# Performance work log

Hardware: AMD Instinct MI355X
Metric: run time of the kernel (lower is better)

## Reference

```python
import jax, jax.numpy as jnp
import numpy as np

N_NODES, N_EDGES, WIDTH = 50000, 640000, 128


def setup_inputs() -> dict:
    key = jax.random.key(0)
    k1, k2, k3 = jax.random.split(key, 3)
    x = jax.random.normal(k1, (N_NODES, WIDTH), dtype=jnp.float32)
    e = jax.random.randint(k2, (2, N_EDGES), 0, N_NODES, dtype=jnp.int32)
    # LinearBlock(2*width, width): Linear(256 -> 128) + ReLU
    W = jax.random.normal(k3, (WIDTH, 2 * WIDTH), dtype=jnp.float32) * (1.0 / np.sqrt(2 * WIDTH))
    b = jnp.zeros((WIDTH,), dtype=jnp.float32)
    return {"x": x, "e": e, "W": W, "b": b}


def reference(x, e, W, b):
    src, dst = e[0], e[1]
    # gather-subtract: diffs[k] = x[dst_k] - x[src_k]  -> [E, width]
    diffs = x[dst] - x[src]
    n = x.shape[0]
    # scatter_max over destination nodes; torch_scatter leaves empty segments at 0
    maxes = jax.ops.segment_max(diffs, dst, num_segments=n)  # [N, width]
    deg = jax.ops.segment_sum(jnp.ones((dst.shape[0],), jnp.float32), dst, num_segments=n)
    maxes = jnp.where((deg > 0)[:, None], maxes, 0.0)
    # LinearBlock (Linear + ReLU) on concat, then residual
    h = jnp.concatenate([x, maxes], axis=1)  # [N, 2*width]
    return x + jax.nn.relu(h @ W.T + b)
```

## Files before the change

### kernel.cpp

```cpp
#include <hip/hip_runtime.h>

#define WIDTH   128
#define NNODES  50000
#define NEDGES  640000
#define NTILES  3125
#define WLDS_STRIDE 264

#define RBLK    8
#define SSEG    8
#define RSZ     6250
#define SEG_I4  20000
#define C0      16
#define CAPB    128

#define BIN_BLOCKS  (RBLK * SSEG)
#define CVT_BLOCKS  782
#define GRID_PREP   (BIN_BLOCKS + CVT_BLOCKS + 1)

typedef __attribute__((ext_vector_type(8))) short         short8;
typedef __attribute__((ext_vector_type(4))) short         short4_t;
typedef __attribute__((ext_vector_type(4))) float         float4_t;
typedef __attribute__((ext_vector_type(8))) _Float16      half8_t;
typedef __attribute__((ext_vector_type(2))) _Float16      h2v;
typedef __attribute__((ext_vector_type(2))) unsigned int  uint2v;

union H8 { short8 s; half8_t h; };

__device__ inline short f2bf(float f) {
    union { float f; unsigned int u; } a;
    a.f = f;
    unsigned int r = a.u + 0x7FFFu + ((a.u >> 16) & 1u);
    return (short)(r >> 16);
}
__device__ inline unsigned int pack2bf(float a, float b) {
    unsigned int lo = (unsigned short)f2bf(a);
    unsigned int hi = (unsigned short)f2bf(b);
    return lo | (hi << 16);
}

__device__ inline unsigned short f2h(float f) {
    _Float16 h = (_Float16)f;
    union { _Float16 h; unsigned short u; } c; c.h = h; return c.u;
}
__device__ inline unsigned int pack2h(float a, float b) {
    return (unsigned)f2h(a) | ((unsigned)f2h(b) << 16);
}
__device__ inline float h2f_lo(unsigned u) {
    union { unsigned short u; _Float16 h; } c; c.u = (unsigned short)(u & 0xFFFFu);
    return (float)c.h;
}
__device__ inline float h2f_hi(unsigned u) {
    union { unsigned short u; _Float16 h; } c; c.u = (unsigned short)(u >> 16);
    return (float)c.h;
}
__device__ inline unsigned hmin2u(unsigned a, unsigned b) {
    union { unsigned u; h2v h; } ca, cb, cr;
    ca.u = a; cb.u = b;
    cr.h = __builtin_elementwise_min(ca.h, cb.h);
    return cr.u;
}

__global__ __launch_bounds__(1024) void prep_kernel(
    const float* __restrict__ x, const int* __restrict__ e,
    const float* __restrict__ W,
    uint4* __restrict__ xh4, uint2* __restrict__ wh2,
    unsigned char* __restrict__ counts8,
    unsigned short* __restrict__ bucketsU)
{
    __shared__ int cnt[RSZ];
    const int bid = blockIdx.x;
    const int tid = threadIdx.x;

    if (bid < BIN_BLOCKS) {
        int r = bid & (RBLK - 1);
        int s = bid >> 3;
        int base = r * RSZ;
        int rsz  = RSZ;

        for (int i = tid; i < RSZ; i += 1024) cnt[i] = 0;
        __syncthreads();

        const int4* dst4 = (const int4*)(e + NEDGES + s * (SEG_I4 * 4));
        const int4* src4 = (const int4*)(e + s * (SEG_I4 * 4));

        int i = tid;
        int4 d = (i < SEG_I4) ? dst4[i] : make_int4(-1, -1, -1, -1);
        while (i < SEG_I4) {
            int inx = i + 1024;
            int4 dn = d;
            if (inx < SEG_I4) dn = dst4[inx];

            unsigned a0 = (unsigned)(d.x - base);
            unsigned a1 = (unsigned)(d.y - base);
            unsigned a2 = (unsigned)(d.z - base);
            unsigned a3 = (unsigned)(d.w - base);
            bool m0 = a0 < (unsigned)rsz;
            bool m1 = a1 < (unsigned)rsz;
            bool m2 = a2 < (unsigned)rsz;
            bool m3 = a3 < (unsigned)rsz;
            if (m0 | m1 | m2 | m3) {
                int4 sv = src4[i];
                if (m0) { int p = atomicAdd(&cnt[a0], 1); if (p < C0) bucketsU[(size_t)d.x * CAPB + s * C0 + p] = (unsigned short)sv.x; }
                if (m1) { int p = atomicAdd(&cnt[a1], 1); if (p < C0) bucketsU[(size_t)d.y * CAPB + s * C0 + p] = (unsigned short)sv.y; }
                if (m2) { int p = atomicAdd(&cnt[a2], 1); if (p < C0) bucketsU[(size_t)d.z * CAPB + s * C0 + p] = (unsigned short)sv.z; }
                if (m3) { int p = atomicAdd(&cnt[a3], 1); if (p < C0) bucketsU[(size_t)d.w * CAPB + s * C0 + p] = (unsigned short)sv.w; }
            }
            d = dn; i = inx;
        }
        __syncthreads();
        for (int i2 = tid; i2 < rsz; i2 += 1024) {
            int c = cnt[i2]; if (c > C0) c = C0;
            counts8[(size_t)(base + i2) * SSEG + s] = (unsigned char)c;
        }
    } else if (bid < BIN_BLOCKS + CVT_BLOCKS) {
        int i = (bid - BIN_BLOCKS) * 1024 + tid;
        if (i < 800000) {
            const float4* xf = (const float4*)x;
            float4 v0 = xf[2 * i];
            float4 v1 = xf[2 * i + 1];
            uint4 p;
            p.x = pack2h(v0.x, v0.y); p.y = pack2h(v0.z, v0.w);
            p.z = pack2h(v1.x, v1.y); p.w = pack2h(v1.z, v1.w);
            xh4[i] = p;
        }
    } else {
        for (int j = tid; j < 8192; j += 1024) {
            float4 v = ((const float4*)W)[j];
            uint2 p; p.x = pack2h(v.x, v.y); p.y = pack2h(v.z, v.w);
            wh2[j] = p;
        }
    }
}

__global__ __launch_bounds__(256) void gather_min_f16_kernel(
    const uint2* __restrict__ xh2,
    const unsigned char* __restrict__ counts8,
    const unsigned int* __restrict__ bucketsU32,
    uint2* __restrict__ maxesh2)
{
    int wave = (blockIdx.x * 256 + threadIdx.x) >> 6;
    int lane = threadIdx.x & 63;
    if (wave >= NNODES) return;
    int node = wave;

    const int gb = lane >> 3;
    const int jj = (lane & 7) * 2;

    const unsigned int* cp = (const unsigned int*)(counts8 + (size_t)node * 8);
    unsigned int ccx = __builtin_nontemporal_load(cp);
    unsigned int ccy = __builtin_nontemporal_load(cp + 1);
    unsigned int u = __builtin_nontemporal_load(bucketsU32 + (size_t)node * 64 + lane);

    unsigned int cg = ((gb < 4 ? ccx : ccy) >> ((gb & 3) * 8)) & 0xFFu;
    bool va = (unsigned)jj < cg;
    bool vb = (unsigned)(jj + 1) < cg;
    unsigned long long ma = __ballot(va);
    unsigned long long mb = __ballot(vb);
    int popcA = __popcll(ma);
    int pA = __builtin_amdgcn_mbcnt_hi((unsigned)(ma >> 32),
              __builtin_amdgcn_mbcnt_lo((unsigned)ma, 0));
    int pB = popcA + __builtin_amdgcn_mbcnt_hi((unsigned)(mb >> 32),
              __builtin_amdgcn_mbcnt_lo((unsigned)mb, 0));
    int rA = __builtin_amdgcn_ds_permute((va ? pA : 63) << 2,
                                         (int)(u & 0xFFFFu));
    int rB = __builtin_amdgcn_ds_permute(((vb && pB < 64) ? pB : 63) << 2,
                                         (int)(u >> 16));
    int deg   = popcA + __popcll(mb);
    int myidx = (lane < popcA) ? rA : rB;

    int h  = lane >> 5;
    int cl = lane & 31;

    unsigned m01 = 0x7BFF7BFFu;
    unsigned m23 = 0x7BFF7BFFu;
#pragma unroll 1
    for (int j0 = 0; j0 < deg; j0 += 16) {
        uint2 v[8];
#pragma unroll
        for (int uu = 0; uu < 8; ++uu) {
            int jc = j0 + 2 * uu + h;
            jc = jc < deg ? jc : deg - 1;
            int src = __shfl(myidx, jc);
            v[uu] = xh2[(size_t)src * 32 + cl];
        }
        unsigned a0 = hmin2u(v[0].x, v[1].x), a1 = hmin2u(v[2].x, v[3].x);
        unsigned a2 = hmin2u(v[4].x, v[5].x), a3 = hmin2u(v[6].x, v[7].x);
        m01 = hmin2u(m01, hmin2u(hmin2u(a0, a1), hmin2u(a2, a3)));
        unsigned b0 = hmin2u(v[0].y, v[1].y), b1 = hmin2u(v[2].y, v[3].y);
        unsigned b2 = hmin2u(v[4].y, v[5].y), b3 = hmin2u(v[6].y, v[7].y);
        m23 = hmin2u(m23, hmin2u(hmin2u(b0, b1), hmin2u(b2, b3)));
    }
    m01 = hmin2u(m01, (unsigned)__shfl_xor((int)m01, 32));
    m23 = hmin2u(m23, (unsigned)__shfl_xor((int)m23, 32));

    if (h == 0) {
        uint2v o;
        if (deg > 0) {
            uint2 xv = xh2[(size_t)node * 32 + cl];
            o.x = pack2h(h2f_lo(xv.x) - h2f_lo(m01), h2f_hi(xv.x) - h2f_hi(m01));
            o.y = pack2h(h2f_lo(xv.y) - h2f_lo(m23), h2f_hi(xv.y) - h2f_hi(m23));
        } else {
            o.x = 0u; o.y = 0u;
        }
        __builtin_nontemporal_store(o, (uint2v*)(maxesh2 + (size_t)node * 32 + cl));
    }
}

__global__ __launch_bounds__(256) void fill_kernel(
    const int* __restrict__ e, int* __restrict__ counts, int* __restrict__ buckets)
{
    int i = blockIdx.x * 256 + threadIdx.x;
    if (i >= NEDGES) return;
    int src = e[i];
    int dst = e[NEDGES + i];
    int pos = atomicAdd(&counts[dst], 1);
    if (pos < 64) buckets[dst * 64 + pos] = src;
}

__global__ __launch_bounds__(256) void gather_min_fp32_kernel(
    const float* __restrict__ x, const int* __restrict__ counts,
    const int* __restrict__ buckets, unsigned int* __restrict__ maxes_u32)
{
    int wave = (blockIdx.x * 256 + threadIdx.x) >> 6;
    int lane = threadIdx.x & 63;
    if (wave >= NNODES) return;
    int node = wave;
    int deg  = counts[node];
    deg = deg > 64 ? 64 : deg;

    int myidx = (lane < deg) ? buckets[node * 64 + lane] : 0;
    int c = lane * 2;
    float2 m; m.x = 3.4e38f; m.y = 3.4e38f;
#pragma unroll 1
    for (int j0 = 0; j0 < deg; j0 += 8) {
        float2 v[8];
#pragma unroll
        for (int u = 0; u < 8; ++u) {
            int jc = j0 + u;
            jc = jc < deg ? jc : deg - 1;
            int src = __shfl(myidx, jc);
            v[u] = *(const float2*)(x + (size_t)src * WIDTH + c);
        }
#pragma unroll
        for (int u = 0; u < 8; ++u) {
            m.x = fminf(m.x, v[u].x);
            m.y = fminf(m.y, v[u].y);
        }
    }
    float2 o;
    if (deg > 0) {
        float2 xv = *(const float2*)(x + (size_t)node * WIDTH + c);
        o.x = xv.x - m.x;
        o.y = xv.y - m.y;
    } else { o.x = 0.f; o.y = 0.f; }
    maxes_u32[(size_t)node * 64 + lane] = pack2bf(o.x, o.y);
}

template<bool FAST>
__global__ __launch_bounds__(256, 2) void fused_gemm_kernel(
    const float* __restrict__ x, const short* __restrict__ xh,
    const short* __restrict__ maxes,
    const float* __restrict__ W, const short* __restrict__ Wh,
    const float* __restrict__ b, float* __restrict__ out)
{
    __shared__ short Wlds[WIDTH * WLDS_STRIDE];

    const int t = threadIdx.x;

    if (FAST) {
#pragma unroll
        for (int i = 0; i < 32; ++i) {
            int idx8 = t + i * 256;
            int flat = idx8 << 3;
            short8 w = *(const short8*)(Wh + flat);
            int n = flat >> 8;
            int k = flat & 255;
            *(short4_t*)&Wlds[n * WLDS_STRIDE + k]     = *(short4_t*)&w;
            *(short4_t*)&Wlds[n * WLDS_STRIDE + k + 4] = *((short4_t*)&w + 1);
        }
    } else {
#pragma unroll
        for (int i = 0; i < 32; ++i) {
            int idx4 = t + i * 256;
            int flat = idx4 << 2;
            float4 w = *(const float4*)(W + flat);
            int n = flat >> 8;
            int k = flat & 255;
            short4_t s;
            s.x = f2bf(w.x); s.y = f2bf(w.y); s.z = f2bf(w.z); s.w = f2bf(w.w);
            *(short4_t*)&Wlds[n * WLDS_STRIDE + k] = s;
        }
    }
    __syncthreads();

    const int wave  = t >> 6;
    const int lane  = t & 63;
    const int lm    = lane & 15;
    const int quad  = lane >> 4;
    const int nhalf = wave & 1;
    const int wpair = wave >> 1;
    const int ncol_base = nhalf * 64;

    short8 bfrag[4][8];
#pragma unroll
    for (int nt = 0; nt < 4; ++nt) {
        int n = ncol_base + nt * 16 + lm;
#pragma unroll
        for (int kt = 0; kt < 8; ++kt) {
            int k = kt * 32 + quad * 8;
            bfrag[nt][kt] = *(const short8*)&Wlds[n * WLDS_STRIDE + k];
        }
    }

    const _Float16* xhf = (const _Float16*)xh;

    const int stride = gridDim.x * 2;
#pragma unroll 1
    for (int tile = blockIdx.x * 2 + wpair; tile < NTILES; tile += stride) {
        int row = tile * 16 + lm;
        const float* xr  = x     + (size_t)row * WIDTH;
        const short* xhr = xh    + (size_t)row * WIDTH;
        const short* mr  = maxes + (size_t)row * WIDTH;

        float4_t acc[4];
#pragma unroll
        for (int nt = 0; nt < 4; ++nt) { acc[nt].x = 0.f; acc[nt].y = 0.f; acc[nt].z = 0.f; acc[nt].w = 0.f; }

#pragma unroll
        for (int kt = 0; kt < 8; ++kt) {
            int k = kt * 32 + quad * 8;
            short8 afrag;
            if (FAST) {
                afrag = (k < WIDTH) ? *(const short8*)(xhr + k)
                                    : *(const short8*)(mr + (k - WIDTH));
            } else {
                if (k < WIDTH) {
                    float4 v0 = *(const float4*)(xr + k);
                    float4 v1 = *(const float4*)(xr + k + 4);
                    afrag[0] = f2bf(v0.x); afrag[1] = f2bf(v0.y);
                    afrag[2] = f2bf(v0.z); afrag[3] = f2bf(v0.w);
                    afrag[4] = f2bf(v1.x); afrag[5] = f2bf(v1.y);
                    afrag[6] = f2bf(v1.z); afrag[7] = f2bf(v1.w);
                } else {
                    afrag = *(const short8*)(mr + (k - WIDTH));
                }
            }
#pragma unroll
            for (int nt = 0; nt < 4; ++nt) {
                if (FAST) {
                    H8 a, bb; a.s = afrag; bb.s = bfrag[nt][kt];
                    acc[nt] = __builtin_amdgcn_mfma_f32_16x16x32_f16(
                        a.h, bb.h, acc[nt], 0, 0, 0);
                } else {
                    acc[nt] = __builtin_amdgcn_mfma_f32_16x16x32_bf16(
                        afrag, bfrag[nt][kt], acc[nt], 0, 0, 0);
                }
            }
        }

#pragma unroll
        for (int nt = 0; nt < 4; ++nt) {
            int col = ncol_base + nt * 16 + lm;
            float bias = b[col];
#pragma unroll
            for (int r = 0; r < 4; ++r) {
                int orow = tile * 16 + quad * 4 + r;
                float v = acc[nt][r] + bias;
                v = v > 0.f ? v : 0.f;
                size_t off = (size_t)orow * WIDTH + col;
                float res = FAST ? (float)xhf[off] : x[off];
                out[off] = res + v;
            }
        }
    }
}

extern "C" void kernel_launch(void* const* d_in, const int* in_sizes, int n_in,
                              void* d_out, int out_size, void* d_ws, size_t ws_size,
                              hipStream_t stream) {
    const float* x = (const float*)d_in[0];
    const int*   e = (const int*)  d_in[1];
    const float* W = (const float*)d_in[2];
    const float* b = (const float*)d_in[3];
    float* out = (float*)d_out;

    char* ws = (char*)d_ws;

    const size_t off_counts  = 64;
    const size_t off_buckets = 400128;
    const size_t off_xh      = off_buckets + 12800000;
    const size_t off_maxesh  = off_xh + 12800000;
    const size_t off_wh      = off_maxesh + 12800000;
    const size_t need        = off_wh + 65536;

    if (ws_size >= need) {
        unsigned char*  counts8  = (unsigned char*)(ws + off_counts);
        unsigned short* bucketsU = (unsigned short*)(ws + off_buckets);
        short*          xh       = (short*)(ws + off_xh);
        short*          maxesh   = (short*)(ws + off_maxesh);
        short*          wh       = (short*)(ws + off_wh);

        prep_kernel<<<GRID_PREP, 1024, 0, stream>>>(
            x, e, W, (uint4*)xh, (uint2*)wh, counts8, bucketsU);
        gather_min_f16_kernel<<<(NNODES + 3) / 4, 256, 0, stream>>>(
            (const uint2*)xh, counts8, (const unsigned int*)bucketsU,
            (uint2*)maxesh);
        fused_gemm_kernel<true><<<512, 256, 0, stream>>>(
            x, xh, maxesh, W, wh, b, out);
    } else {
        int*          counts  = (int*)ws;
        int*          buckets = (int*)(ws + 262144);
        unsigned int* maxes   = (unsigned int*)(ws + 262144 + 12800000);

        (void)hipMemsetAsync(counts, 0, 262144, stream);
        fill_kernel<<<(NEDGES + 255) / 256, 256, 0, stream>>>(e, counts, buckets);
        gather_min_fp32_kernel<<<(NNODES + 3) / 4, 256, 0, stream>>>(
            x, counts, buckets, maxes);
        fused_gemm_kernel<false><<<512, 256, 0, stream>>>(
            x, nullptr, (const short*)maxes, W, nullptr, b, out);
    }
}
```

Before: 150.7 us.

## Fuse neighbor gather-min with GEMM, keeping maxes tile in LDS

Merges the per-node gather/min kernel and the MFMA GEMM into one kernel. Each 512-thread block gathers 64 nodes into a shared-memory tile, then eight waves run the 256->128 GEMM on that tile, so the 12.8 MB maxes buffer is never written to or read back from global memory and one launch goes away. In exchange, W fragments are now read from global memory (L2) on every block rather than held in registers, and the GEMM phase cannot start until the block's slowest gather finishes.

```diff
diff --git a/kernel.cpp b/kernel.cpp
--- a/kernel.cpp
+++ b/kernel.cpp
@@ -4,7 +4,6 @@
 #define NNODES  50000
 #define NEDGES  640000
 #define NTILES  3125
-#define WLDS_STRIDE 264
 
 #define RBLK    8
 #define SSEG    8
@@ -16,6 +15,10 @@
 #define BIN_BLOCKS  (RBLK * SSEG)
 #define CVT_BLOCKS  782
 #define GRID_PREP   (BIN_BLOCKS + CVT_BLOCKS + 1)
+
+#define FUSE_ROWS   64
+#define FUSE_BLOCKS 782
+#define MLDS_STRIDE 264
 
 typedef __attribute__((ext_vector_type(8))) short         short8;
 typedef __attribute__((ext_vector_type(4))) short         short4_t;
@@ -132,77 +135,133 @@
     }
 }
 
-__global__ __launch_bounds__(256) void gather_min_f16_kernel(
+__global__ __launch_bounds__(512, 4) void fused_gather_gemm_kernel(
     const uint2* __restrict__ xh2,
     const unsigned char* __restrict__ counts8,
     const unsigned int* __restrict__ bucketsU32,
-    uint2* __restrict__ maxesh2)
+    const short* __restrict__ xh, const short* __restrict__ Wh,
+    const float* __restrict__ b, float* __restrict__ out)
 {
-    int wave = (blockIdx.x * 256 + threadIdx.x) >> 6;
-    int lane = threadIdx.x & 63;
-    if (wave >= NNODES) return;
-    int node = wave;
+    __shared__ short Mlds[FUSE_ROWS * MLDS_STRIDE];
+
+    const int tid  = threadIdx.x;
+    const int wave = tid >> 6;
+    const int lane = tid & 63;
+    const int base = blockIdx.x * FUSE_ROWS;
 
     const int gb = lane >> 3;
     const int jj = (lane & 7) * 2;
-
-    const unsigned int* cp = (const unsigned int*)(counts8 + (size_t)node * 8);
-    unsigned int ccx = __builtin_nontemporal_load(cp);
-    unsigned int ccy = __builtin_nontemporal_load(cp + 1);
-    unsigned int u = __builtin_nontemporal_load(bucketsU32 + (size_t)node * 64 + lane);
-
-    unsigned int cg = ((gb < 4 ? ccx : ccy) >> ((gb & 3) * 8)) & 0xFFu;
-    bool va = (unsigned)jj < cg;
-    bool vb = (unsigned)(jj + 1) < cg;
-    unsigned long long ma = __ballot(va);
-    unsigned long long mb = __ballot(vb);
-    int popcA = __popcll(ma);
-    int pA = __builtin_amdgcn_mbcnt_hi((unsigned)(ma >> 32),
-              __builtin_amdgcn_mbcnt_lo((unsigned)ma, 0));
-    int pB = popcA + __builtin_amdgcn_mbcnt_hi((unsigned)(mb >> 32),
-              __builtin_amdgcn_mbcnt_lo((unsigned)mb, 0));
-    int rA = __builtin_amdgcn_ds_permute((va ? pA : 63) << 2,
-                                         (int)(u & 0xFFFFu));
-    int rB = __builtin_amdgcn_ds_permute(((vb && pB < 64) ? pB : 63) << 2,
-                                         (int)(u >> 16));
-    int deg   = popcA + __popcll(mb);
-    int myidx = (lane < popcA) ? rA : rB;
-
-    int h  = lane >> 5;
-    int cl = lane & 31;
-
-    unsigned m01 = 0x7BFF7BFFu;
-    unsigned m23 = 0x7BFF7BFFu;
+    const int h  = lane >> 5;
+    const int cl = lane & 31;
+
 #pragma unroll 1
-    for (int j0 = 0; j0 < deg; j0 += 16) {
-        uint2 v[8];
-#pragma unroll
-        for (int uu = 0; uu < 8; ++uu) {
-            int jc = j0 + 2 * uu + h;
-            jc = jc < deg ? jc : deg - 1;
-            int src = __shfl(myidx, jc);
-            v[uu] = xh2[(size_t)src * 32 + cl];
-        }
-        unsigned a0 = hmin2u(v[0].x, v[1].x), a1 = hmin2u(v[2].x, v[3].x);
-        unsigned a2 = hmin2u(v[4].x, v[5].x), a3 = hmin2u(v[6].x, v[7].x);
-        m01 = hmin2u(m01, hmin2u(hmin2u(a0, a1), hmin2u(a2, a3)));
-        unsigned b0 = hmin2u(v[0].y, v[1].y), b1 = hmin2u(v[2].y, v[3].y);
-        unsigned b2 = hmin2u(v[4].y, v[5].y), b3 = hmin2u(v[6].y, v[7].y);
-        m23 = hmin2u(m23, hmin2u(hmin2u(b0, b1), hmin2u(b2, b3)));
-    }
-    m01 = hmin2u(m01, (unsigned)__shfl_xor((int)m01, 32));
-    m23 = hmin2u(m23, (unsigned)__shfl_xor((int)m23, 32));
-
-    if (h == 0) {
-        uint2v o;
-        if (deg > 0) {
-            uint2 xv = xh2[(size_t)node * 32 + cl];
-            o.x = pack2h(h2f_lo(xv.x) - h2f_lo(m01), h2f_hi(xv.x) - h2f_hi(m01));
-            o.y = pack2h(h2f_lo(xv.y) - h2f_lo(m23), h2f_hi(xv.y) - h2f_hi(m23));
-        } else {
-            o.x = 0u; o.y = 0u;
-        }
-        __builtin_nontemporal_store(o, (uint2v*)(maxesh2 + (size_t)node * 32 + cl));
+    for (int r = 0; r < 8; ++r) {
+        int node = base + wave * 8 + r;
+        if (node < NNODES) {
+            const unsigned int* cp = (const unsigned int*)(counts8 + (size_t)node * 8);
+            unsigned int ccx = __builtin_nontemporal_load(cp);
+            unsigned int ccy = __builtin_nontemporal_load(cp + 1);
+            unsigned int u = __builtin_nontemporal_load(bucketsU32 + (size_t)node * 64 + lane);
+
+            unsigned int cg = ((gb < 4 ? ccx : ccy) >> ((gb & 3) * 8)) & 0xFFu;
+            bool va = (unsigned)jj < cg;
+            bool vb = (unsigned)(jj + 1) < cg;
+            unsigned long long ma = __ballot(va);
+            unsigned long long mb = __ballot(vb);
+            int popcA = __popcll(ma);
+            int pA = __builtin_amdgcn_mbcnt_hi((unsigned)(ma >> 32),
+                      __builtin_amdgcn_mbcnt_lo((unsigned)ma, 0));
+            int pB = popcA + __builtin_amdgcn_mbcnt_hi((unsigned)(mb >> 32),
+                      __builtin_amdgcn_mbcnt_lo((unsigned)mb, 0));
+            int rA = __builtin_amdgcn_ds_permute((va ? pA : 63) << 2,
+                                                 (int)(u & 0xFFFFu));
+            int rB = __builtin_amdgcn_ds_permute(((vb && pB < 64) ? pB : 63) << 2,
+                                                 (int)(u >> 16));
+            int deg   = popcA + __popcll(mb);
+            int myidx = (lane < popcA) ? rA : rB;
+
+            unsigned m01 = 0x7BFF7BFFu;
+            unsigned m23 = 0x7BFF7BFFu;
+#pragma unroll 1
+            for (int j0 = 0; j0 < deg; j0 += 16) {
+                uint2 v[8];
+#pragma unroll
+                for (int uu = 0; uu < 8; ++uu) {
+                    int jc = j0 + 2 * uu + h;
+                    jc = jc < deg ? jc : deg - 1;
+                    int src = __shfl(myidx, jc);
+                    v[uu] = xh2[(size_t)src * 32 + cl];
+                }
+                unsigned a0 = hmin2u(v[0].x, v[1].x), a1 = hmin2u(v[2].x, v[3].x);
+                unsigned a2 = hmin2u(v[4].x, v[5].x), a3 = hmin2u(v[6].x, v[7].x);
+                m01 = hmin2u(m01, hmin2u(hmin2u(a0, a1), hmin2u(a2, a3)));
+                unsigned b0 = hmin2u(v[0].y, v[1].y), b1 = hmin2u(v[2].y, v[3].y);
+                unsigned b2 = hmin2u(v[4].y, v[5].y), b3 = hmin2u(v[6].y, v[7].y);
+                m23 = hmin2u(m23, hmin2u(hmin2u(b0, b1), hmin2u(b2, b3)));
+            }
+            m01 = hmin2u(m01, (unsigned)__shfl_xor((int)m01, 32));
+            m23 = hmin2u(m23, (unsigned)__shfl_xor((int)m23, 32));
+
+            if (h == 0) {
+                uint2 o;
+                if (deg > 0) {
+                    uint2 xv = xh2[(size_t)node * 32 + cl];
+                    o.x = pack2h(h2f_lo(xv.x) - h2f_lo(m01), h2f_hi(xv.x) - h2f_hi(m01));
+                    o.y = pack2h(h2f_lo(xv.y) - h2f_lo(m23), h2f_hi(xv.y) - h2f_hi(m23));
+                } else {
+                    o.x = 0u; o.y = 0u;
+                }
+                *(uint2*)&Mlds[(wave * 8 + r) * MLDS_STRIDE + cl * 4] = o;
+            }
+        }
+    }
+    __syncthreads();
+
+    const int lm    = lane & 15;
+    const int quad  = lane >> 4;
+    const int nhalf = wave & 1;
+    const int wpair = wave >> 1;
+    const int ncol_base = nhalf * 64;
+
+    int trow = base + wpair * 16;
+    if (trow < NNODES) {
+        int row = trow + lm;
+        const short* xhr   = xh + (size_t)row * WIDTH;
+        const short* mldsr = &Mlds[(wpair * 16 + lm) * MLDS_STRIDE];
+        const _Float16* xhf = (const _Float16*)xh;
+
+        float4_t acc[4];
+#pragma unroll
+        for (int nt = 0; nt < 4; ++nt) { acc[nt].x = 0.f; acc[nt].y = 0.f; acc[nt].z = 0.f; acc[nt].w = 0.f; }
+
+#pragma unroll 1
+        for (int kt = 0; kt < 8; ++kt) {
+            int k = kt * 32 + quad * 8;
+            short8 afrag = (k < WIDTH) ? *(const short8*)(xhr + k)
+                                       : *(const short8*)(mldsr + (k - WIDTH));
+#pragma unroll
+            for (int nt = 0; nt < 4; ++nt) {
+                int n = ncol_base + nt * 16 + lm;
+                short8 bfrag = *(const short8*)(Wh + (size_t)n * 256 + k);
+                H8 a, bb; a.s = afrag; bb.s = bfrag;
+                acc[nt] = __builtin_amdgcn_mfma_f32_16x16x32_f16(
+                    a.h, bb.h, acc[nt], 0, 0, 0);
+            }
+        }
+
+#pragma unroll
+        for (int nt = 0; nt < 4; ++nt) {
+            int col = ncol_base + nt * 16 + lm;
+            float bias = b[col];
+#pragma unroll
+            for (int r = 0; r < 4; ++r) {
+                int orow = trow + quad * 4 + r;
+                float v = acc[nt][r] + bias;
+                v = v > 0.f ? v : 0.f;
+                size_t off = (size_t)orow * WIDTH + col;
+                out[off] = (float)xhf[off] + v;
+            }
+        }
     }
 }
 
@@ -256,40 +315,24 @@
     maxes_u32[(size_t)node * 64 + lane] = pack2bf(o.x, o.y);
 }
 
-template<bool FAST>
-__global__ __launch_bounds__(256, 2) void fused_gemm_kernel(
-    const float* __restrict__ x, const short* __restrict__ xh,
-    const short* __restrict__ maxes,
-    const float* __restrict__ W, const short* __restrict__ Wh,
-    const float* __restrict__ b, float* __restrict__ out)
+__global__ __launch_bounds__(256, 2) void fused_gemm_fb_kernel(
+    const float* __restrict__ x, const short* __restrict__ maxes,
+    const float* __restrict__ W, const float* __restrict__ b,
+    float* __restrict__ out)
 {
-    __shared__ short Wlds[WIDTH * WLDS_STRIDE];
+    __shared__ short Wlds[WIDTH * MLDS_STRIDE];
 
     const int t = threadIdx.x;
-
-    if (FAST) {
-#pragma unroll
-        for (int i = 0; i < 32; ++i) {
-            int idx8 = t + i * 256;
-            int flat = idx8 << 3;
-            short8 w = *(const short8*)(Wh + flat);
-            int n = flat >> 8;
-            int k = flat & 255;
-            *(short4_t*)&Wlds[n * WLDS_STRIDE + k]     = *(short4_t*)&w;
-            *(short4_t*)&Wlds[n * WLDS_STRIDE + k + 4] = *((short4_t*)&w + 1);
-        }
-    } else {
-#pragma unroll
-        for (int i = 0; i < 32; ++i) {
-            int idx4 = t + i * 256;
-            int flat = idx4 << 2;
-            float4 w = *(const float4*)(W + flat);
-            int n = flat >> 8;
-            int k = flat & 255;
-            short4_t s;
-            s.x = f2bf(w.x); s.y = f2bf(w.y); s.z = f2bf(w.z); s.w = f2bf(w.w);
-            *(short4_t*)&Wlds[n * WLDS_STRIDE + k] = s;
-        }
+#pragma unroll
+    for (int i = 0; i < 32; ++i) {
+        int idx4 = t + i * 256;
+        int flat = idx4 << 2;
+        float4 w = *(const float4*)(W + flat);
+        int n = flat >> 8;
+        int k = flat & 255;
+        short4_t s;
+        s.x = f2bf(w.x); s.y = f2bf(w.y); s.z = f2bf(w.z); s.w = f2bf(w.w);
+        *(short4_t*)&Wlds[n * MLDS_STRIDE + k] = s;
     }
     __syncthreads();
 
@@ -308,19 +351,16 @@
 #pragma unroll
         for (int kt = 0; kt < 8; ++kt) {
             int k = kt * 32 + quad * 8;
-            bfrag[nt][kt] = *(const short8*)&Wlds[n * WLDS_STRIDE + k];
-        }
-    }
-
-    const _Float16* xhf = (const _Float16*)xh;
+            bfrag[nt][kt] = *(const short8*)&Wlds[n * MLDS_STRIDE + k];
+        }
+    }
 
     const int stride = gridDim.x * 2;
 #pragma unroll 1
     for (int tile = blockIdx.x * 2 + wpair; tile < NTILES; tile += stride) {
         int row = tile * 16 + lm;
-        const float* xr  = x     + (size_t)row * WIDTH;
-        const short* xhr = xh    + (size_t)row * WIDTH;
-        const short* mr  = maxes + (size_t)row * WIDTH;
+        const float* xr = x     + (size_t)row * WIDTH;
+        const short* mr = maxes + (size_t)row * WIDTH;
 
         float4_t acc[4];
 #pragma unroll
@@ -330,31 +370,20 @@
         for (int kt = 0; kt < 8; ++kt) {
             int k = kt * 32 + quad * 8;
             short8 afrag;
-            if (FAST) {
-                afrag = (k < WIDTH) ? *(const short8*)(xhr + k)
-                                    : *(const short8*)(mr + (k - WIDTH));
+            if (k < WIDTH) {
+                float4 v0 = *(const float4*)(xr + k);
+                float4 v1 = *(const float4*)(xr + k + 4);
+                afrag[0] = f2bf(v0.x); afrag[1] = f2bf(v0.y);
+                afrag[2] = f2bf(v0.z); afrag[3] = f2bf(v0.w);
+                afrag[4] = f2bf(v1.x); afrag[5] = f2bf(v1.y);
+                afrag[6] = f2bf(v1.z); afrag[7] = f2bf(v1.w);
             } else {
-                if (k < WIDTH) {
-                    float4 v0 = *(const float4*)(xr + k);
-                    float4 v1 = *(const float4*)(xr + k + 4);
-                    afrag[0] = f2bf(v0.x); afrag[1] = f2bf(v0.y);
-                    afrag[2] = f2bf(v0.z); afrag[3] = f2bf(v0.w);
-                    afrag[4] = f2bf(v1.x); afrag[5] = f2bf(v1.y);
-                    afrag[6] = f2bf(v1.z); afrag[7] = f2bf(v1.w);
-                } else {
-                    afrag = *(const short8*)(mr + (k - WIDTH));
-                }
+                afrag = *(const short8*)(mr + (k - WIDTH));
             }
 #pragma unroll
             for (int nt = 0; nt < 4; ++nt) {
-                if (FAST) {
-                    H8 a, bb; a.s = afrag; bb.s = bfrag[nt][kt];
-                    acc[nt] = __builtin_amdgcn_mfma_f32_16x16x32_f16(
-                        a.h, bb.h, acc[nt], 0, 0, 0);
-                } else {
-                    acc[nt] = __builtin_amdgcn_mfma_f32_16x16x32_bf16(
-                        afrag, bfrag[nt][kt], acc[nt], 0, 0, 0);
-                }
+                acc[nt] = __builtin_amdgcn_mfma_f32_16x16x32_bf16(
+                    afrag, bfrag[nt][kt], acc[nt], 0, 0, 0);
             }
         }
 
@@ -368,8 +397,7 @@
                 float v = acc[nt][r] + bias;
                 v = v > 0.f ? v : 0.f;
                 size_t off = (size_t)orow * WIDTH + col;
-                float res = FAST ? (float)xhf[off] : x[off];
-                out[off] = res + v;
+                out[off] = x[off] + v;
             }
         }
     }
@@ -389,24 +417,20 @@
     const size_t off_counts  = 64;
     const size_t off_buckets = 400128;
     const size_t off_xh      = off_buckets + 12800000;
-    const size_t off_maxesh  = off_xh + 12800000;
-    const size_t off_wh      = off_maxesh + 12800000;
+    const size_t off_wh      = off_xh + 12800000;
     const size_t need        = off_wh + 65536;
 
     if (ws_size >= need) {
         unsigned char*  counts8  = (unsigned char*)(ws + off_counts);
         unsigned short* bucketsU = (unsigned short*)(ws + off_buckets);
         short*          xh       = (short*)(ws + off_xh);
-        short*          maxesh   = (short*)(ws + off_maxesh);
         short*          wh       = (short*)(ws + off_wh);
 
         prep_kernel<<<GRID_PREP, 1024, 0, stream>>>(
             x, e, W, (uint4*)xh, (uint2*)wh, counts8, bucketsU);
-        gather_min_f16_kernel<<<(NNODES + 3) / 4, 256, 0, stream>>>(
+        fused_gather_gemm_kernel<<<FUSE_BLOCKS, 512, 0, stream>>>(
             (const uint2*)xh, counts8, (const unsigned int*)bucketsU,
-            (uint2*)maxesh);
-        fused_gemm_kernel<true><<<512, 256, 0, stream>>>(
-            x, xh, maxesh, W, wh, b, out);
+            xh, wh, b, out);
     } else {
         int*          counts  = (int*)ws;
         int*          buckets = (int*)(ws + 262144);
@@ -416,7 +440,7 @@
         fill_kernel<<<(NEDGES + 255) / 256, 256, 0, stream>>>(e, counts, buckets);
         gather_min_fp32_kernel<<<(NNODES + 3) / 4, 256, 0, stream>>>(
             x, counts, buckets, maxes);
-        fused_gemm_kernel<false><<<512, 256, 0, stream>>>(
-            x, nullptr, (const short*)maxes, W, nullptr, b, out);
-    }
-}
+        fused_gemm_fb_kernel<<<512, 256, 0, stream>>>(
+            x, (const short*)maxes, W, b, out);
+    }
+}
```

New measurement: 168.9 us. 12.1% more time.
